# Kernel tuning notes

Hardware: AMD Instinct MI355X
Metric: run time of the kernel (lower is better)

The kernel has to match this reference:

```python
import jax, jax.numpy as jnp
import numpy as np

IN_FEATURES = 11008
OUT_FEATURES = 4096
TOPK = 5504            # in_features * topk_ratio (0.5)
RECALL_THRES = 0.9
N_CACHE = 64           # modeled steady-state cache size


def setup_inputs() -> dict:
    key = jax.random.key(0)
    k1, k2, k3, k4 = jax.random.split(key, 4)
    x = jax.random.normal(k1, (1, 1, IN_FEATURES), dtype=jnp.float32)
    weight = jax.random.normal(k2, (OUT_FEATURES, IN_FEATURES), dtype=jnp.float32) * 0.02
    bias = jax.random.normal(k3, (OUT_FEATURES,), dtype=jnp.float32) * 0.02
    cached_indices = jax.random.randint(k4, (N_CACHE, TOPK), 0, IN_FEATURES, dtype=jnp.int64)
    return {"x": x, "weight": weight, "bias": bias, "cached_indices": cached_indices}


def reference(x, weight, bias, cached_indices):
    # decode path: bsz == seq == 1
    xf = x.reshape(-1, IN_FEATURES)                       # [1, in]
    x_mean = jnp.abs(xf).mean(axis=0)                     # [in]
    # top-k neuron selection (argsort descending -> top_k)
    _, topk_idx = jax.lax.top_k(x_mean, TOPK)             # [topk]
    topk_mask = jnp.zeros((IN_FEATURES,), dtype=bool).at[topk_idx].set(True)
    # rebuild cached boolean masks from cached index sets
    cached_masks = (
        jnp.zeros((N_CACHE, IN_FEATURES), dtype=bool)
        .at[jnp.arange(N_CACHE)[:, None], cached_indices]
        .set(True)
    )
    # recall of each cached mask against current top-k mask
    intersection = jnp.sum(cached_masks & topk_mask[None, :], axis=1)  # [n_cache]
    recalls = intersection.astype(jnp.float32) / TOPK
    best_idx = jnp.argmax(recalls)
    best_recall = recalls[best_idx]
    # cache hit -> reuse cached indices; miss -> use fresh top-k indices
    idx = jnp.where(best_recall >= RECALL_THRES, cached_indices[best_idx], topk_idx)
    # gather sparse column slice, then small GEMM + bias
    w_slice = weight[:, idx]                               # [out, topk]
    out = xf[:, idx] @ w_slice.T + bias                    # [1, out]
    return out.reshape(1, 1, OUT_FEATURES)
```

## Files before the change

### kernel.cpp

```cpp
#include <hip/hip_runtime.h>
#include <stdint.h>

#define IN_F   11008
#define OUT_F  4096
#define TOPK_K 5504
#define NCACHE 64
#define MASK_WORDS 344
#define NTHR   512
#define NCHUNK 22
#define ROWS_PER_BLOCK 16
#define NWORK  (OUT_F / ROWS_PER_BLOCK)
#define NBLK   (1 + NWORK)


__device__ __forceinline__ unsigned absbits(float v) {
    return __float_as_uint(v) & 0x7fffffffu;
}

__global__ __launch_bounds__(NTHR, 4) void k_all(const float* __restrict__ x,
                                                 const float* __restrict__ W,
                                                 const float* __restrict__ bias,
                                                 const int* __restrict__ cached,
                                                 float* __restrict__ out,
                                                 unsigned* __restrict__ maskbits_g,
                                                 unsigned* __restrict__ score_g,
                                                 unsigned* __restrict__ flag_g,
                                                 unsigned* __restrict__ done_g) {
    __shared__ unsigned hist[8][256];
    __shared__ unsigned csum[256];
    __shared__ unsigned sh_T, sh_rem, sh_totEq;
    __shared__ unsigned waveEq[NCHUNK][8];
    __shared__ unsigned waveEqPre[NCHUNK][8];
    __shared__ unsigned rowbits[MASK_WORDS];
    __shared__ unsigned wsum[8];
    __shared__ __align__(16) float xs[IN_F];

    const int tid  = threadIdx.x;
    const int wv   = tid >> 6;
    const int lane = tid & 63;
    const int bid  = blockIdx.x;

    if (bid == 0) {
        {
            float4* xs4w = (float4*)xs;
#pragma unroll
            for (int k = 0; k < 6; ++k) {
                int j = k * NTHR + tid;
                if (j < IN_F / 4) xs4w[j] = ((const float4*)x)[j];
            }
        }
        __syncthreads();

        const int nk = (tid < 256) ? NCHUNK : NCHUNK - 1;

        unsigned key[NCHUNK];
#pragma unroll
        for (int c = 0; c < NCHUNK; ++c) {
            key[c] = 0u;
            if (c < nk) key[c] = absbits(xs[c * NTHR + tid]);
        }
        __syncthreads();

        unsigned prefix = 0, maskHi = 0, remaining = TOPK_K;

        for (int pass = 3; pass >= 0; --pass) {
            const int sh = pass * 8;
            for (int b = tid; b < 8 * 256; b += NTHR) ((unsigned*)hist)[b] = 0;
            __syncthreads();
#pragma unroll
            for (int c = 0; c < NCHUNK; ++c) {
                if (c < nk && (key[c] & maskHi) == prefix)
                    atomicAdd(&hist[wv][(key[c] >> sh) & 255], 1u);
            }
            __syncthreads();
            if (tid < 256) {
                unsigned s = 0;
#pragma unroll
                for (int w = 0; w < 8; ++w) s += hist[w][tid];
                csum[tid] = s;
            }
            __syncthreads();
            if (wv == 0) {
                unsigned c0 = csum[4 * lane + 0], c1 = csum[4 * lane + 1];
                unsigned c2 = csum[4 * lane + 2], c3 = csum[4 * lane + 3];
                unsigned S = c0 + c1 + c2 + c3;
#pragma unroll
                for (int off = 1; off < 64; off <<= 1) {
                    unsigned v = __shfl_down(S, off, 64);
                    if (lane + off < 64) S += v;
                }
                unsigned Sn = __shfl_down(S, 1, 64);
                if (lane == 63) Sn = 0;
                unsigned t3 = Sn + c3;
                unsigned t2 = t3 + c2;
                unsigned t1 = t2 + c1;
                unsigned t0 = t1 + c0;
                unsigned rem = remaining;
                if (t3 >= rem && Sn < rem) { sh_T = prefix | ((unsigned)(4 * lane + 3) << sh); sh_rem = rem - Sn; }
                if (t2 >= rem && t3 < rem) { sh_T = prefix | ((unsigned)(4 * lane + 2) << sh); sh_rem = rem - t3; }
                if (t1 >= rem && t2 < rem) { sh_T = prefix | ((unsigned)(4 * lane + 1) << sh); sh_rem = rem - t2; }
                if (t0 >= rem && t1 < rem) { sh_T = prefix | ((unsigned)(4 * lane + 0) << sh); sh_rem = rem - t1; }
            }
            __syncthreads();
            prefix = sh_T;
            maskHi |= 0xffu << sh;
            remaining = sh_rem;
        }

        const unsigned T = prefix;
        const unsigned eqTake = remaining;

        unsigned gtm = 0, eqm = 0;
#pragma unroll
        for (int c = 0; c < NCHUNK; ++c) {
            if (c < nk) {
                if (key[c] > T)       gtm |= 1u << c;
                else if (key[c] == T) eqm |= 1u << c;
            }
        }
#pragma unroll
        for (int c = 0; c < NCHUNK; ++c) {
            unsigned long long bal = __ballot((eqm >> c) & 1u);
            if (lane == 0) waveEq[c][wv] = (unsigned)__popcll(bal);
        }
        __syncthreads();
        if (tid < 64) {
            unsigned s = 0;
            for (int p = lane; p < NCHUNK * 8; p += 64) s += waveEq[p >> 3][p & 7];
#pragma unroll
            for (int off = 32; off > 0; off >>= 1) s += __shfl_down(s, off, 64);
            if (lane == 0) sh_totEq = s;
        }
        __syncthreads();
        const bool fast = (sh_totEq == eqTake);
        if (!fast) {
            if (tid == 0) {
                unsigned run = 0;
                for (int c = 0; c < NCHUNK; ++c)
                    for (int w = 0; w < 8; ++w) { waveEqPre[c][w] = run; run += waveEq[c][w]; }
            }
            __syncthreads();
        }
#pragma unroll
        for (int c = 0; c < NCHUNK; ++c) {
            bool eq = (eqm >> c) & 1u;
            bool take;
            if (fast) {
                take = (((gtm >> c) & 1u) != 0u) || eq;
            } else {
                unsigned long long balEq = __ballot(eq);
                unsigned rank = waveEqPre[c][wv] + (unsigned)__popcll(balEq & ((1ull << lane) - 1ull));
                take = (((gtm >> c) & 1u) != 0u) || (eq && rank < eqTake);
            }
            unsigned long long balT = __ballot(take);
            int w0 = c * 16 + wv * 2;
            if (w0 < MASK_WORDS && lane == 0) {
                maskbits_g[w0]     = (unsigned)balT;
                maskbits_g[w0 + 1] = (unsigned)(balT >> 32);
            }
        }
        __syncthreads();
        if (tid == 0) {
            __threadfence();
            __hip_atomic_store(flag_g, 1u, __ATOMIC_RELEASE, __HIP_MEMORY_SCOPE_AGENT);
        }
        return;
    }

    const int g = bid - 1;
    const float4* wp = (const float4*)(W + (size_t)g * (ROWS_PER_BLOCK * IN_F));
    const bool doRecall = (g < NCACHE);

    if (doRecall) {
        for (int w = tid; w < MASK_WORDS; w += NTHR) rowbits[w] = 0;
        __syncthreads();
        const int4* ci4 = (const int4*)(cached + (size_t)g * TOPK_K);
        for (int t = tid; t < TOPK_K / 4; t += NTHR) {
            int4 v = ci4[t];
            atomicOr(&rowbits[v.x >> 5], 1u << (v.x & 31));
            atomicOr(&rowbits[v.y >> 5], 1u << (v.y & 31));
            atomicOr(&rowbits[v.z >> 5], 1u << (v.z & 31));
            atomicOr(&rowbits[v.w >> 5], 1u << (v.w & 31));
        }
        __syncthreads();
    }

    {
        const int NCH = (ROWS_PER_BLOCK * IN_F / 4) / (2 * NTHR);
        for (int c = 0; c < NCH; ++c) {
            if (c >= 1 && __hip_atomic_load(flag_g, __ATOMIC_RELAXED, __HIP_MEMORY_SCOPE_AGENT) != 0u)
                break;
            float4 a = wp[c * 2 * NTHR + tid];
            float4 b = wp[c * 2 * NTHR + NTHR + tid];
            asm volatile("" :: "v"(a.x), "v"(a.y), "v"(a.z), "v"(a.w));
            asm volatile("" :: "v"(b.x), "v"(b.y), "v"(b.z), "v"(b.w));
        }
    }

    if (tid == 0) {
        while (__hip_atomic_load(flag_g, __ATOMIC_ACQUIRE, __HIP_MEMORY_SCOPE_AGENT) == 0u)
            __builtin_amdgcn_s_sleep(8);
    }
    __syncthreads();

    if (doRecall) {
        unsigned cnt = 0;
        for (int w = tid; w < MASK_WORDS; w += NTHR) cnt += __popc(rowbits[w] & maskbits_g[w]);
        for (int off = 32; off > 0; off >>= 1) cnt += __shfl_down(cnt, off, 64);
        if (lane == 0) wsum[wv] = cnt;
        __syncthreads();
        if (tid == 0) {
            unsigned tot = 0;
#pragma unroll
            for (int w = 0; w < 8; ++w) tot += wsum[w];
            atomicMax(score_g, (tot << 6) | (unsigned)(63 - g));
            __hip_atomic_fetch_add(done_g, 1u, __ATOMIC_RELEASE, __HIP_MEMORY_SCOPE_AGENT);
        }
    }

    {
        const float4* x4 = (const float4*)x;
        for (int j = tid; j < IN_F / 4; j += NTHR) {
            float4 xv = x4[j];
            int base = j * 4;
            unsigned wbits = maskbits_g[base >> 5];
            int sh = base & 31;
            xs[base + 0] = xv.x * (float)((wbits >> (sh + 0)) & 1u);
            xs[base + 1] = xv.y * (float)((wbits >> (sh + 1)) & 1u);
            xs[base + 2] = xv.z * (float)((wbits >> (sh + 2)) & 1u);
            xs[base + 3] = xv.w * (float)((wbits >> (sh + 3)) & 1u);
        }
    }
    __syncthreads();

    const int row0 = g * ROWS_PER_BLOCK + wv * 2;
    const int row1 = row0 + 1;
    const float4* w0p = (const float4*)(W + (size_t)row0 * IN_F);
    const float4* w1p = (const float4*)(W + (size_t)row1 * IN_F);
    const float4* xs4 = (const float4*)xs;

    float acc0 = 0.f, acc1 = 0.f;
#pragma unroll 4
    for (int j = lane; j < IN_F / 4; j += 64) {
        float4 xv = xs4[j];
        float4 a  = w0p[j];
        float4 b  = w1p[j];
        acc0 += xv.x * a.x + xv.y * a.y + xv.z * a.z + xv.w * a.w;
        acc1 += xv.x * b.x + xv.y * b.y + xv.z * b.z + xv.w * b.w;
    }
    for (int off = 32; off > 0; off >>= 1) {
        acc0 += __shfl_down(acc0, off, 64);
        acc1 += __shfl_down(acc1, off, 64);
    }

    if (tid == 0) {
        while (__hip_atomic_load(done_g, __ATOMIC_ACQUIRE, __HIP_MEMORY_SCOPE_AGENT) < NCACHE)
            __builtin_amdgcn_s_sleep(2);
    }
    __syncthreads();

    unsigned score = *score_g;
    bool useCache = ((float)(score >> 6) / (float)TOPK_K) >= 0.9f;
    if (!useCache) {
        if (lane == 0) {
            out[row0] = acc0 + bias[row0];
            out[row1] = acc1 + bias[row1];
        }
    } else {
        int best = 63 - (int)(score & 63u);
        __syncthreads();
        for (int i = tid; i < IN_F; i += NTHR) xs[i] = 0.f;
        __syncthreads();
        const int* ci = cached + (size_t)best * TOPK_K;
        for (int t = tid; t < TOPK_K; t += NTHR) {
            int idx = ci[t];
            atomicAdd(&xs[idx], x[idx]);
        }
        __syncthreads();
        float a0 = 0.f, a1 = 0.f;
#pragma unroll 4
        for (int j = lane; j < IN_F / 4; j += 64) {
            float4 xv = xs4[j];
            float4 a  = w0p[j];
            float4 b  = w1p[j];
            a0 += xv.x * a.x + xv.y * a.y + xv.z * a.z + xv.w * a.w;
            a1 += xv.x * b.x + xv.y * b.y + xv.z * b.z + xv.w * b.w;
        }
        for (int off = 32; off > 0; off >>= 1) {
            a0 += __shfl_down(a0, off, 64);
            a1 += __shfl_down(a1, off, 64);
        }
        if (lane == 0) {
            out[row0] = a0 + bias[row0];
            out[row1] = a1 + bias[row1];
        }
    }
}

extern "C" void kernel_launch(void* const* d_in, const int* in_sizes, int n_in,
                              void* d_out, int out_size, void* d_ws, size_t ws_size,
                              hipStream_t stream) {
    const float* x      = (const float*)d_in[0];
    const float* W      = (const float*)d_in[1];
    const float* bias   = (const float*)d_in[2];
    const int*   cached = (const int*)d_in[3];
    float* out = (float*)d_out;

    char* ws = (char*)d_ws;
    unsigned* maskbits = (unsigned*)(ws + 0);
    unsigned* score    = (unsigned*)(ws + 1472);
    unsigned* flag     = (unsigned*)(ws + 1476);
    unsigned* done     = (unsigned*)(ws + 1480);

    hipMemsetAsync(ws + 1472, 0, 12, stream);
    k_all<<<NBLK, NTHR, 0, stream>>>(x, W, bias, cached, out,
                                     maskbits, score, flag, done);
}
```

Measured before the change: 264.3 us.

## Publish top-k threshold early and mask x by threshold inside GEMV

Block 0 now publishes the radix-select threshold T and a fast-path flag before it writes the mask bits, and signals mask completion through a separate flag. GEMV blocks can start as soon as T is known: they mask x on the fly by comparing absolute bits against T instead of waiting for the bitmask and building a masked copy in shared memory. They fall back to the bitmask path only when ties make the threshold ambiguous. The weight prefetch loop is also restructured into larger batches of loads, which adds a second flag and extra control-flow complexity.

```diff
diff --git a/kernel.cpp b/kernel.cpp
--- a/kernel.cpp
+++ b/kernel.cpp
@@ -25,7 +25,9 @@
                                                  unsigned* __restrict__ maskbits_g,
                                                  unsigned* __restrict__ score_g,
                                                  unsigned* __restrict__ flag_g,
-                                                 unsigned* __restrict__ done_g) {
+                                                 unsigned* __restrict__ done_g,
+                                                 unsigned* __restrict__ maskflag_g,
+                                                 unsigned* __restrict__ Tval_g) {
     __shared__ unsigned hist[8][256];
     __shared__ unsigned csum[256];
     __shared__ unsigned sh_T, sh_rem, sh_totEq;
@@ -33,6 +35,7 @@
     __shared__ unsigned waveEqPre[NCHUNK][8];
     __shared__ unsigned rowbits[MASK_WORDS];
     __shared__ unsigned wsum[8];
+    __shared__ unsigned sh_flagv, sh_Tv;
     __shared__ __align__(16) float xs[IN_F];
 
     const int tid  = threadIdx.x;
@@ -133,6 +136,14 @@
         }
         __syncthreads();
         const bool fast = (sh_totEq == eqTake);
+
+        if (tid == 0) {
+            *Tval_g = T;
+            __threadfence();
+            __hip_atomic_store(flag_g, 1u | (fast ? 2u : 0u),
+                               __ATOMIC_RELEASE, __HIP_MEMORY_SCOPE_AGENT);
+        }
+
         if (!fast) {
             if (tid == 0) {
                 unsigned run = 0;
@@ -162,7 +173,7 @@
         __syncthreads();
         if (tid == 0) {
             __threadfence();
-            __hip_atomic_store(flag_g, 1u, __ATOMIC_RELEASE, __HIP_MEMORY_SCOPE_AGENT);
+            __hip_atomic_store(maskflag_g, 1u, __ATOMIC_RELEASE, __HIP_MEMORY_SCOPE_AGENT);
         }
         return;
     }
@@ -186,24 +197,63 @@
     }
 
     {
-        const int NCH = (ROWS_PER_BLOCK * IN_F / 4) / (2 * NTHR);
-        for (int c = 0; c < NCH; ++c) {
-            if (c >= 1 && __hip_atomic_load(flag_g, __ATOMIC_RELAXED, __HIP_MEMORY_SCOPE_AGENT) != 0u)
-                break;
-            float4 a = wp[c * 2 * NTHR + tid];
-            float4 b = wp[c * 2 * NTHR + NTHR + tid];
-            asm volatile("" :: "v"(a.x), "v"(a.y), "v"(a.z), "v"(a.w));
-            asm volatile("" :: "v"(b.x), "v"(b.y), "v"(b.z), "v"(b.w));
+        bool stop = false;
+        for (int r = 0; r < 10; ++r) {
+            if (r > 0 && __hip_atomic_load(flag_g, __ATOMIC_RELAXED, __HIP_MEMORY_SCOPE_AGENT) != 0u) {
+                stop = true; break;
+            }
+            const int base = r * 4096;
+            float4 a0 = wp[base +    0 + tid];
+            float4 a1 = wp[base +  512 + tid];
+            float4 a2 = wp[base + 1024 + tid];
+            float4 a3 = wp[base + 1536 + tid];
+            float4 a4 = wp[base + 2048 + tid];
+            float4 a5 = wp[base + 2560 + tid];
+            float4 a6 = wp[base + 3072 + tid];
+            float4 a7 = wp[base + 3584 + tid];
+            asm volatile("" :: "v"(a0.x), "v"(a0.y), "v"(a0.z), "v"(a0.w));
+            asm volatile("" :: "v"(a1.x), "v"(a1.y), "v"(a1.z), "v"(a1.w));
+            asm volatile("" :: "v"(a2.x), "v"(a2.y), "v"(a2.z), "v"(a2.w));
+            asm volatile("" :: "v"(a3.x), "v"(a3.y), "v"(a3.z), "v"(a3.w));
+            asm volatile("" :: "v"(a4.x), "v"(a4.y), "v"(a4.z), "v"(a4.w));
+            asm volatile("" :: "v"(a5.x), "v"(a5.y), "v"(a5.z), "v"(a5.w));
+            asm volatile("" :: "v"(a6.x), "v"(a6.y), "v"(a6.z), "v"(a6.w));
+            asm volatile("" :: "v"(a7.x), "v"(a7.y), "v"(a7.z), "v"(a7.w));
+        }
+        if (!stop && __hip_atomic_load(flag_g, __ATOMIC_RELAXED, __HIP_MEMORY_SCOPE_AGENT) == 0u) {
+            const int base = 40960;
+            float4 a0 = wp[base +    0 + tid];
+            float4 a1 = wp[base +  512 + tid];
+            float4 a2 = wp[base + 1024 + tid];
+            float4 a3 = wp[base + 1536 + tid];
+            float4 a4 = wp[base + 2048 + tid];
+            float4 a5 = wp[base + 2560 + tid];
+            asm volatile("" :: "v"(a0.x), "v"(a0.y), "v"(a0.z), "v"(a0.w));
+            asm volatile("" :: "v"(a1.x), "v"(a1.y), "v"(a1.z), "v"(a1.w));
+            asm volatile("" :: "v"(a2.x), "v"(a2.y), "v"(a2.z), "v"(a2.w));
+            asm volatile("" :: "v"(a3.x), "v"(a3.y), "v"(a3.z), "v"(a3.w));
+            asm volatile("" :: "v"(a4.x), "v"(a4.y), "v"(a4.z), "v"(a4.w));
+            asm volatile("" :: "v"(a5.x), "v"(a5.y), "v"(a5.z), "v"(a5.w));
         }
     }
 
     if (tid == 0) {
-        while (__hip_atomic_load(flag_g, __ATOMIC_ACQUIRE, __HIP_MEMORY_SCOPE_AGENT) == 0u)
+        unsigned f;
+        while ((f = __hip_atomic_load(flag_g, __ATOMIC_ACQUIRE, __HIP_MEMORY_SCOPE_AGENT)) == 0u)
             __builtin_amdgcn_s_sleep(8);
+        sh_flagv = f;
+        sh_Tv = *Tval_g;
     }
     __syncthreads();
+    const bool fastSel = (sh_flagv & 2u) != 0u;
+    const unsigned Tv  = sh_Tv;
 
     if (doRecall) {
+        if (tid == 0) {
+            while (__hip_atomic_load(maskflag_g, __ATOMIC_ACQUIRE, __HIP_MEMORY_SCOPE_AGENT) == 0u)
+                __builtin_amdgcn_s_sleep(4);
+        }
+        __syncthreads();
         unsigned cnt = 0;
         for (int w = tid; w < MASK_WORDS; w += NTHR) cnt += __popc(rowbits[w] & maskbits_g[w]);
         for (int off = 32; off > 0; off >>= 1) cnt += __shfl_down(cnt, off, 64);
@@ -218,31 +268,20 @@
         }
     }
 
-    {
-        const float4* x4 = (const float4*)x;
-        for (int j = tid; j < IN_F / 4; j += NTHR) {
-            float4 xv = x4[j];
-            int base = j * 4;
-            unsigned wbits = maskbits_g[base >> 5];
-            int sh = base & 31;
-            xs[base + 0] = xv.x * (float)((wbits >> (sh + 0)) & 1u);
-            xs[base + 1] = xv.y * (float)((wbits >> (sh + 1)) & 1u);
-            xs[base + 2] = xv.z * (float)((wbits >> (sh + 2)) & 1u);
-            xs[base + 3] = xv.w * (float)((wbits >> (sh + 3)) & 1u);
-        }
-    }
-    __syncthreads();
-
     const int row0 = g * ROWS_PER_BLOCK + wv * 2;
     const int row1 = row0 + 1;
     const float4* w0p = (const float4*)(W + (size_t)row0 * IN_F);
     const float4* w1p = (const float4*)(W + (size_t)row1 * IN_F);
-    const float4* xs4 = (const float4*)xs;
+    const float4* x4g = (const float4*)x;
 
     float acc0 = 0.f, acc1 = 0.f;
 #pragma unroll 4
     for (int j = lane; j < IN_F / 4; j += 64) {
-        float4 xv = xs4[j];
+        float4 xv = x4g[j];
+        xv.x = (absbits(xv.x) >= Tv) ? xv.x : 0.f;
+        xv.y = (absbits(xv.y) >= Tv) ? xv.y : 0.f;
+        xv.z = (absbits(xv.z) >= Tv) ? xv.z : 0.f;
+        xv.w = (absbits(xv.w) >= Tv) ? xv.w : 0.f;
         float4 a  = w0p[j];
         float4 b  = w1p[j];
         acc0 += xv.x * a.x + xv.y * a.y + xv.z * a.z + xv.w * a.w;
@@ -261,22 +300,43 @@
 
     unsigned score = *score_g;
     bool useCache = ((float)(score >> 6) / (float)TOPK_K) >= 0.9f;
-    if (!useCache) {
+    bool redo = useCache || !fastSel;
+    if (!redo) {
         if (lane == 0) {
             out[row0] = acc0 + bias[row0];
             out[row1] = acc1 + bias[row1];
         }
     } else {
-        int best = 63 - (int)(score & 63u);
-        __syncthreads();
-        for (int i = tid; i < IN_F; i += NTHR) xs[i] = 0.f;
-        __syncthreads();
-        const int* ci = cached + (size_t)best * TOPK_K;
-        for (int t = tid; t < TOPK_K; t += NTHR) {
-            int idx = ci[t];
-            atomicAdd(&xs[idx], x[idx]);
-        }
-        __syncthreads();
+        const float4* xs4 = (const float4*)xs;
+        __syncthreads();
+        if (useCache) {
+            int best = 63 - (int)(score & 63u);
+            for (int i = tid; i < IN_F; i += NTHR) xs[i] = 0.f;
+            __syncthreads();
+            const int* ci = cached + (size_t)best * TOPK_K;
+            for (int t = tid; t < TOPK_K; t += NTHR) {
+                int idx = ci[t];
+                atomicAdd(&xs[idx], x[idx]);
+            }
+            __syncthreads();
+        } else {
+            if (tid == 0) {
+                while (__hip_atomic_load(maskflag_g, __ATOMIC_ACQUIRE, __HIP_MEMORY_SCOPE_AGENT) == 0u)
+                    __builtin_amdgcn_s_sleep(4);
+            }
+            __syncthreads();
+            for (int j = tid; j < IN_F / 4; j += NTHR) {
+                float4 xv = x4g[j];
+                int base = j * 4;
+                unsigned wbits = maskbits_g[base >> 5];
+                int sh = base & 31;
+                xs[base + 0] = xv.x * (float)((wbits >> (sh + 0)) & 1u);
+                xs[base + 1] = xv.y * (float)((wbits >> (sh + 1)) & 1u);
+                xs[base + 2] = xv.z * (float)((wbits >> (sh + 2)) & 1u);
+                xs[base + 3] = xv.w * (float)((wbits >> (sh + 3)) & 1u);
+            }
+            __syncthreads();
+        }
         float a0 = 0.f, a1 = 0.f;
 #pragma unroll 4
         for (int j = lane; j < IN_F / 4; j += 64) {
@@ -311,8 +371,10 @@
     unsigned* score    = (unsigned*)(ws + 1472);
     unsigned* flag     = (unsigned*)(ws + 1476);
     unsigned* done     = (unsigned*)(ws + 1480);
-
-    hipMemsetAsync(ws + 1472, 0, 12, stream);
+    unsigned* maskflag = (unsigned*)(ws + 1484);
+    unsigned* Tval     = (unsigned*)(ws + 1488);
+
+    hipMemsetAsync(ws + 1472, 0, 16, stream);
     k_all<<<NBLK, NTHR, 0, stream>>>(x, W, bias, cached, out,
-                                     maskbits, score, flag, done);
+                                     maskbits, score, flag, done, maskflag, Tval);
 }
```

Measured after the change: 264.3 us. About the same (+0.0%).
